# Kernel optimization log

Measured on AMD Instinct MI355X. Metric: run time of the kernel, lower is better.

## Reference

```python
import jax, jax.numpy as jnp
import numpy as np

N = 20000   # nodes
E = 200000  # directed edges (~kNN k=5, bidirectional)
IN = 256    # in_channels
D = 512     # projected_channels = in_channels * 2
NEG_SLOPE = 0.2


def _ln(x, g, b):
    mu = x.mean(-1, keepdims=True)
    var = ((x - mu) ** 2).mean(-1, keepdims=True)
    return (x - mu) * jax.lax.rsqrt(var + 1e-5) * g + b


def _gat(x, src, dst, W, a_s, a_d, bias, concat):
    # PyG GATConv: linear -> per-edge leaky-relu attention -> segment softmax over dst -> scatter-add
    n = x.shape[0]
    H, C = a_s.shape
    h = (x @ W).reshape(n, H, C)                      # [N,H,C]
    as_n = jnp.einsum('nhc,hc->nh', h, a_s)           # alpha contribution of src node
    ad_n = jnp.einsum('nhc,hc->nh', h, a_d)           # alpha contribution of dst node
    e = jax.nn.leaky_relu(as_n[src] + ad_n[dst], negative_slope=NEG_SLOPE)  # [E,H]
    m = jax.ops.segment_max(e, dst, num_segments=n)   # stable softmax per dst (self-loops => every dst nonempty)
    ex = jnp.exp(e - m[dst])
    den = jax.ops.segment_sum(ex, dst, num_segments=n)
    alpha = ex / den[dst]                             # [E,H]
    out = jax.ops.segment_sum(h[src] * alpha[:, :, None], dst, num_segments=n)  # [N,H,C]
    out = out.reshape(n, H * C) if concat else out.mean(axis=1)
    return out + bias


def setup_inputs() -> dict:
    key = jax.random.key(0)
    ks = jax.random.split(key, 40)
    x = jax.random.normal(ks[0], (N, IN), jnp.float32)
    src = jax.random.randint(ks[1], (E,), 0, N)
    off = jax.random.randint(ks[2], (E,), 1, N)
    dst = (src + off) % N                              # guarantees src != dst
    edge_index = jnp.stack([src, dst]).astype(jnp.int64)

    def p(k, shape, fan):
        return (jax.random.normal(k, shape, jnp.float32) / np.float32(np.sqrt(fan)))

    inp = {
        'x': x, 'edge_index': edge_index,
        'proj_W': p(ks[3], (IN, D), IN), 'proj_b': jnp.zeros((D,), jnp.float32),
        'blk_norm_g': jnp.ones((3, D), jnp.float32), 'blk_norm_b': jnp.zeros((3, D), jnp.float32),
        'g1_W': p(ks[4], (3, D, D), D), 'g1_as': p(ks[5], (3, 4, 128), 128), 'g1_ad': p(ks[6], (3, 4, 128), 128),
        'g1_b': jnp.zeros((3, D), jnp.float32),
        'g2_W': p(ks[7], (3, D, 128), D), 'g2_as': p(ks[8], (3, 2, 64), 64), 'g2_ad': p(ks[9], (3, 2, 64), 64),
        'g2_b': jnp.zeros((3, 128), jnp.float32),
        'uni_W': p(ks[10], (3, 640, D), 640), 'uni_b': jnp.zeros((3, D), jnp.float32),
        'fin_g': jnp.ones((D,), jnp.float32), 'fin_b': jnp.zeros((D,), jnp.float32),
        'fg_W': p(ks[11], (D, 8 * 128), D), 'fg_as': p(ks[12], (8, 128), 128), 'fg_ad': p(ks[13], (8, 128), 128),
        'fg_b': jnp.zeros((128,), jnp.float32),
    }
    return inp


def reference(x, edge_index, proj_W, proj_b, blk_norm_g, blk_norm_b,
              g1_W, g1_as, g1_ad, g1_b, g2_W, g2_as, g2_ad, g2_b,
              uni_W, uni_b, fin_g, fin_b, fg_W, fg_as, fg_ad, fg_b):
    n = x.shape[0]
    loops = jnp.arange(n, dtype=edge_index.dtype)
    src = jnp.concatenate([edge_index[0], loops])     # add_self_loops (PyG default)
    dst = jnp.concatenate([edge_index[1], loops])

    x = jax.nn.elu(x @ proj_W + proj_b)
    for i in range(3):
        res = x
        xn = _ln(x, blk_norm_g[i], blk_norm_b[i])
        o1 = _gat(xn, src, dst, g1_W[i], g1_as[i], g1_ad[i], g1_b[i], True)
        o2 = _gat(xn, src, dst, g2_W[i], g2_as[i], g2_ad[i], g2_b[i], True)
        xc = jax.nn.elu(jnp.concatenate([o1, o2], axis=-1))
        x = res + xc @ uni_W[i] + uni_b[i]
        x = jax.nn.elu(x)
    x = _ln(x, fin_g, fin_b)
    return _gat(x, src, dst, fg_W, fg_as, fg_ad, fg_b, False)  # heads=8, concat=False -> mean
```

## Files before the change

### kernel.cpp

```cpp
#include <hip/hip_runtime.h>
#include <math.h>

#define NN 20000
#define EDGES 200000

using short8  = __attribute__((ext_vector_type(8))) short;
using short4v = __attribute__((ext_vector_type(4))) short;
using f32x4   = __attribute__((ext_vector_type(4))) float;
typedef unsigned short ushortT;
typedef unsigned int uintT;

__device__ __forceinline__ ushortT f2bfu(float x) {
  union { float f; unsigned u; } c; c.f = x;
  unsigned r = c.u + 0x7FFFu + ((c.u >> 16) & 1u);
  return (ushortT)(r >> 16);
}
__device__ __forceinline__ float bflo(uintT u) {
  union { unsigned i; float f; } c; c.i = u << 16; return c.f;
}
__device__ __forceinline__ float bfhi(uintT u) {
  union { unsigned i; float f; } c; c.i = u & 0xFFFF0000u; return c.f;
}
__device__ __forceinline__ float elu_f(float v) { return v > 0.f ? v : (expf(v) - 1.f); }

__device__ __forceinline__ void acc8(float* acc, uint4 u, float a) {
  acc[0] += a * bflo(u.x); acc[1] += a * bfhi(u.x);
  acc[2] += a * bflo(u.y); acc[3] += a * bfhi(u.y);
  acc[4] += a * bflo(u.z); acc[5] += a * bfhi(u.z);
  acc[6] += a * bflo(u.w); acc[7] += a * bfhi(u.w);
}

__global__ void k_hist(const int* __restrict__ ei, int* __restrict__ cnt) {
  int i = blockIdx.x * 256 + threadIdx.x;
  const int EE = EDGES + NN;
  if (i >= EE) return;
  int d = (i < EDGES) ? ei[EDGES + i] : (i - EDGES);
  atomicAdd(&cnt[d], 1);
}

__global__ __launch_bounds__(256) void k_scan1(const int* __restrict__ cnt,
                                               int* __restrict__ bsum, int n) {
  int b = blockIdx.x, t = threadIdx.x, i = b * 256 + t;
  int v = (i < n) ? cnt[i] : 0;
#pragma unroll
  for (int off = 32; off > 0; off >>= 1) v += __shfl_down(v, off);
  __shared__ int s[4];
  if ((t & 63) == 0) s[t >> 6] = v;
  __syncthreads();
  if (t == 0) bsum[b] = s[0] + s[1] + s[2] + s[3];
}

__global__ void k_scan2(const int* __restrict__ bsum, int* __restrict__ boff,
                        int nb, int* __restrict__ ptr, int n) {
  if (threadIdx.x == 0) {
    int acc = 0;
    for (int b = 0; b < nb; ++b) { boff[b] = acc; acc += bsum[b]; }
    ptr[n] = acc;
  }
}

__global__ __launch_bounds__(256) void k_scan3(const int* __restrict__ cnt,
                                               const int* __restrict__ boff,
                                               int* __restrict__ ptr,
                                               int* __restrict__ cursor, int n) {
  __shared__ int sd[256];
  int b = blockIdx.x, t = threadIdx.x, i = b * 256 + t;
  int v = (i < n) ? cnt[i] : 0;
  sd[t] = v;
  __syncthreads();
  for (int off = 1; off < 256; off <<= 1) {
    int a = (t >= off) ? sd[t - off] : 0;
    __syncthreads();
    sd[t] += a;
    __syncthreads();
  }
  if (i < n) {
    int p = boff[b] + sd[t] - v;
    ptr[i] = p;
    cursor[i] = p;
  }
}

__global__ void k_scatter(const int* __restrict__ ei, int* __restrict__ cursor,
                          int* __restrict__ ssrc) {
  int i = blockIdx.x * 256 + threadIdx.x;
  const int EE = EDGES + NN;
  if (i >= EE) return;
  int s, d;
  if (i < EDGES) { s = ei[i]; d = ei[EDGES + i]; }
  else           { s = i - EDGES; d = s; }
  int pos = atomicAdd(&cursor[d], 1);
  ssrc[pos] = s;
}

struct CvtDesc { const float* src; ushortT* dst; int K; int N; int t0; };
struct CvtArgs { CvtDesc d[11]; };

__global__ __launch_bounds__(256) void k_cvtT(CvtArgs a) {
  __shared__ float tile[32][33];
  int b = blockIdx.x;
  int mi = 0;
#pragma unroll
  for (int i = 1; i < 11; ++i)
    if (b >= a.d[i].t0) mi = i;
  CvtDesc dd = a.d[mi];
  int tb = b - dd.t0;
  int tnc = dd.N / 32;
  int tk = tb / tnc, tn = tb % tnc;
  int t = threadIdx.x;
  {
    int r = t >> 3, c4 = (t & 7) * 4;
    float4 v = *reinterpret_cast<const float4*>(&dd.src[(size_t)(tk * 32 + r) * dd.N + tn * 32 + c4]);
    tile[r][c4 + 0] = v.x; tile[r][c4 + 1] = v.y; tile[r][c4 + 2] = v.z; tile[r][c4 + 3] = v.w;
  }
  __syncthreads();
  {
    int n = t >> 3, k4 = (t & 7) * 4;
    short4v s;
    s.x = (short)f2bfu(tile[k4 + 0][n]);
    s.y = (short)f2bfu(tile[k4 + 1][n]);
    s.z = (short)f2bfu(tile[k4 + 2][n]);
    s.w = (short)f2bfu(tile[k4 + 3][n]);
    *reinterpret_cast<short4v*>(&dd.dst[(size_t)(tn * 32 + n) * dd.K + tk * 32 + k4]) = s;
  }
}

__global__ void k_cvtX(const float* __restrict__ in, ushortT* __restrict__ out, int n4) {
  int i = blockIdx.x * 256 + threadIdx.x;
  if (i >= n4) return;
  float4 v = reinterpret_cast<const float4*>(in)[i];
  short4v s;
  s.x = (short)f2bfu(v.x); s.y = (short)f2bfu(v.y);
  s.z = (short)f2bfu(v.z); s.w = (short)f2bfu(v.w);
  reinterpret_cast<short4v*>(out)[i] = s;
}

__global__ __launch_bounds__(256) void k_ln(const float* __restrict__ in,
                                            const float* __restrict__ g,
                                            const float* __restrict__ b,
                                            ushortT* __restrict__ out) {
  int row = blockIdx.x, t = threadIdx.x;
  const float* r = in + (size_t)row * 512;
  float v0 = r[t], v1 = r[t + 256];
  __shared__ float red[4];
  int w = t >> 6, lane = t & 63;
  float s = v0 + v1;
#pragma unroll
  for (int off = 32; off > 0; off >>= 1) s += __shfl_down(s, off);
  if (lane == 0) red[w] = s;
  __syncthreads();
  float mu = (red[0] + red[1] + red[2] + red[3]) * (1.f / 512.f);
  float d0 = v0 - mu, d1 = v1 - mu;
  float vs = d0 * d0 + d1 * d1;
#pragma unroll
  for (int off = 32; off > 0; off >>= 1) vs += __shfl_down(vs, off);
  __syncthreads();
  if (lane == 0) red[w] = vs;
  __syncthreads();
  float var = (red[0] + red[1] + red[2] + red[3]) * (1.f / 512.f);
  float rs = rsqrtf(var + 1e-5f);
  ushortT* o = out + (size_t)row * 512;
  o[t]       = f2bfu(d0 * rs * g[t]       + b[t]);
  o[t + 256] = f2bfu(d1 * rs * g[t + 256] + b[t + 256]);
}

template <int EPI, bool OUTBF16, int NB>
__global__ __launch_bounds__(256) void k_gemm(const ushortT* __restrict__ A,
                                              const ushortT* __restrict__ Wt,
                                              const float* __restrict__ bias,
                                              const float* __restrict__ res,
                                              void* __restrict__ Outv,
                                              int M, int N, int K) {
  __shared__ short As[128][40];
  __shared__ short Bs[128][40];
  int b = blockIdx.x;
  int x = b & 7, g = b >> 3;
  int mt = x + 8 * (g / NB);
  int nt = g % NB;
  int m0 = mt * 128, n0 = nt * 128;
  if (m0 >= M) return;
  int t = threadIdx.x;
  int w = t >> 6, lane = t & 63;
  int wm = w >> 1, wn = w & 1;
  int lr = lane & 15, lk = (lane >> 4) * 8;
  int sr = t >> 2, sc = (t & 3) * 8;
  int ga0 = m0 + sr, ga1 = m0 + sr + 64;
  const short8 z8 = {};

  short8 vA0, vA1, vB0, vB1;
  {
    vA0 = (ga0 < M) ? *reinterpret_cast<const short8*>(&A[(size_t)ga0 * K + sc]) : z8;
    vA1 = (ga1 < M) ? *reinterpret_cast<const short8*>(&A[(size_t)ga1 * K + sc]) : z8;
    vB0 = *reinterpret_cast<const short8*>(&Wt[(size_t)(n0 + sr) * K + sc]);
    vB1 = *reinterpret_cast<const short8*>(&Wt[(size_t)(n0 + sr + 64) * K + sc]);
  }
  f32x4 acc[4][4] = {};
  for (int k0 = 0; k0 < K; k0 += 32) {
    *reinterpret_cast<short8*>(&As[sr][sc]) = vA0;
    *reinterpret_cast<short8*>(&As[sr + 64][sc]) = vA1;
    *reinterpret_cast<short8*>(&Bs[sr][sc]) = vB0;
    *reinterpret_cast<short8*>(&Bs[sr + 64][sc]) = vB1;
    __syncthreads();
    int k1 = k0 + 32;
    if (k1 < K) {
      vA0 = (ga0 < M) ? *reinterpret_cast<const short8*>(&A[(size_t)ga0 * K + k1 + sc]) : z8;
      vA1 = (ga1 < M) ? *reinterpret_cast<const short8*>(&A[(size_t)ga1 * K + k1 + sc]) : z8;
      vB0 = *reinterpret_cast<const short8*>(&Wt[(size_t)(n0 + sr) * K + k1 + sc]);
      vB1 = *reinterpret_cast<const short8*>(&Wt[(size_t)(n0 + sr + 64) * K + k1 + sc]);
    }
    short8 af[4], bf[4];
#pragma unroll
    for (int m = 0; m < 4; ++m)
      af[m] = *reinterpret_cast<const short8*>(&As[wm * 64 + m * 16 + lr][lk]);
#pragma unroll
    for (int n = 0; n < 4; ++n)
      bf[n] = *reinterpret_cast<const short8*>(&Bs[wn * 64 + n * 16 + lr][lk]);
#pragma unroll
    for (int m = 0; m < 4; ++m)
#pragma unroll
      for (int n = 0; n < 4; ++n)
        acc[m][n] = __builtin_amdgcn_mfma_f32_16x16x32_bf16(af[m], bf[n], acc[m][n], 0, 0, 0);
    __syncthreads();
  }
#pragma unroll
  for (int m = 0; m < 4; ++m) {
#pragma unroll
    for (int n = 0; n < 4; ++n) {
#pragma unroll
      for (int j = 0; j < 4; ++j) {
        int row = wm * 64 + m * 16 + (lane >> 4) * 4 + j;
        int col = wn * 64 + n * 16 + lr;
        int gr = m0 + row, gc = n0 + col;
        if (gr < M) {
          float v = acc[m][n][j];
          if (EPI >= 1) v += bias[gc];
          if (EPI == 2) v += res[(size_t)gr * N + gc];
          if (EPI >= 1) v = elu_f(v);
          if (OUTBF16) ((ushortT*)Outv)[(size_t)gr * N + gc] = f2bfu(v);
          else         ((float*)Outv)[(size_t)gr * N + gc] = v;
        }
      }
    }
  }
}

__global__ __launch_bounds__(384) void k_att_blk(const ushortT* __restrict__ h,
                                                 const float* __restrict__ w1s,
                                                 const float* __restrict__ w1d,
                                                 const float* __restrict__ w2s,
                                                 const float* __restrict__ w2d,
                                                 float* __restrict__ as_n,
                                                 float* __restrict__ ad_n) {
  int n = blockIdx.x;
  int hh = threadIdx.x >> 6, lane = threadIdx.x & 63;
  float s = 0.f, d = 0.f;
  if (hh < 4) {
    int c = lane * 2;
    uintT u = *reinterpret_cast<const uintT*>(&h[(size_t)n * 640 + hh * 128 + c]);
    float lo = bflo(u), hi = bfhi(u);
    s = lo * w1s[hh * 128 + c] + hi * w1s[hh * 128 + c + 1];
    d = lo * w1d[hh * 128 + c] + hi * w1d[hh * 128 + c + 1];
  } else if (lane < 32) {
    int hb = hh - 4;
    int c = lane * 2;
    uintT u = *reinterpret_cast<const uintT*>(&h[(size_t)n * 640 + 512 + hb * 64 + c]);
    float lo = bflo(u), hi = bfhi(u);
    s = lo * w2s[hb * 64 + c] + hi * w2s[hb * 64 + c + 1];
    d = lo * w2d[hb * 64 + c] + hi * w2d[hb * 64 + c + 1];
  }
#pragma unroll
  for (int o = 32; o > 0; o >>= 1) {
    s += __shfl_down(s, o);
    d += __shfl_down(d, o);
  }
  if (lane == 0) {
    as_n[n * 6 + hh] = s;
    ad_n[n * 6 + hh] = d;
  }
}

template <int H, int C>
__global__ void k_att(const ushortT* __restrict__ h, int rs, int off,
                      const float* __restrict__ as_w,
                      const float* __restrict__ ad_w, float* __restrict__ as_n,
                      float* __restrict__ ad_n) {
  int n = blockIdx.x;
  int hh = threadIdx.x >> 6;
  int lane = threadIdx.x & 63;
  float s = 0.f, d = 0.f;
  if (C == 128 || lane < 32) {
    int c = lane * 2;
    uintT u = *reinterpret_cast<const uintT*>(&h[(size_t)n * rs + off + hh * C + c]);
    float lo = bflo(u), hi = bfhi(u);
    s = lo * as_w[hh * C + c] + hi * as_w[hh * C + c + 1];
    d = lo * ad_w[hh * C + c] + hi * ad_w[hh * C + c + 1];
  }
#pragma unroll
  for (int o = 32; o > 0; o >>= 1) {
    s += __shfl_down(s, o);
    d += __shfl_down(d, o);
  }
  if (lane == 0) {
    as_n[n * H + hh] = s;
    ad_n[n * H + hh] = d;
  }
}

template <int H>
__global__ __launch_bounds__(256) void k_soft16(const float* __restrict__ as_n,
                                                const float* __restrict__ ad_n,
                                                const int* __restrict__ rowptr,
                                                const int* __restrict__ ssrc,
                                                float* __restrict__ alpha) {
  int t = threadIdx.x;
  int grp16 = t >> 4;
  int l = t & 15;
  int dnode = blockIdx.x * 16 + grp16;
  int e0 = rowptr[dnode], deg = rowptr[dnode + 1] - e0;
  float adv[H], m[H], den[H];
#pragma unroll
  for (int hh = 0; hh < H; ++hh) {
    adv[hh] = ad_n[dnode * H + hh];
    m[hh] = -INFINITY;
    den[hh] = 0.f;
  }
  for (int base = 0; base < deg; base += 16) {
    int j = base + l;
    float e[H];
    if (j < deg) {
      int s = ssrc[e0 + j];
#pragma unroll
      for (int hh = 0; hh < H; ++hh) {
        float v = as_n[s * H + hh] + adv[hh];
        e[hh] = v > 0.f ? v : 0.2f * v;
      }
    } else {
#pragma unroll
      for (int hh = 0; hh < H; ++hh) e[hh] = -INFINITY;
    }
#pragma unroll
    for (int hh = 0; hh < H; ++hh) {
      float v = e[hh];
#pragma unroll
      for (int o = 8; o > 0; o >>= 1) v = fmaxf(v, __shfl_xor(v, o, 16));
      m[hh] = fmaxf(m[hh], v);
    }
  }
  for (int base = 0; base < deg; base += 16) {
    int j = base + l;
    float p[H];
    if (j < deg) {
      int s = ssrc[e0 + j];
#pragma unroll
      for (int hh = 0; hh < H; ++hh) {
        float v = as_n[s * H + hh] + adv[hh];
        v = v > 0.f ? v : 0.2f * v;
        p[hh] = expf(v - m[hh]);
        alpha[(size_t)(e0 + j) * H + hh] = p[hh];
      }
    } else {
#pragma unroll
      for (int hh = 0; hh < H; ++hh) p[hh] = 0.f;
    }
#pragma unroll
    for (int hh = 0; hh < H; ++hh) {
      float v = p[hh];
#pragma unroll
      for (int o = 8; o > 0; o >>= 1) v += __shfl_xor(v, o, 16);
      den[hh] += v;
    }
  }
  float rden[H];
#pragma unroll
  for (int hh = 0; hh < H; ++hh) rden[hh] = 1.f / den[hh];
  for (int base = 0; base < deg; base += 16) {
    int j = base + l;
    if (j < deg) {
#pragma unroll
      for (int hh = 0; hh < H; ++hh)
        alpha[(size_t)(e0 + j) * H + hh] *= rden[hh];
    }
  }
}

__global__ __launch_bounds__(320) void k_agg_blk(const ushortT* __restrict__ h,
                                                 const float* __restrict__ alpha,
                                                 const int* __restrict__ rowptr,
                                                 const int* __restrict__ ssrc,
                                                 const float* __restrict__ b1,
                                                 const float* __restrict__ b2,
                                                 ushortT* __restrict__ out) {
  int dnode = blockIdx.x;
  int t = threadIdx.x;
  int grp = t / 80;
  int r = t - grp * 80;
  int ch0 = r * 8;
  int head = (ch0 < 512) ? (ch0 >> 7) : (4 + ((ch0 - 512) >> 6));
  int e0 = rowptr[dnode], deg = rowptr[dnode + 1] - e0;
  float acc[8] = {};
  __shared__ float s_alpha[64 * 6];
  __shared__ int s_src[64];
  __shared__ float s_part[4][640];
  for (int base = 0; base < deg; base += 64) {
    int cnt = min(64, deg - base);
    __syncthreads();
    for (int tix = t; tix < cnt * 6; tix += 320)
      s_alpha[tix] = alpha[(size_t)(e0 + base) * 6 + tix];
    for (int tix = t; tix < cnt; tix += 320)
      s_src[tix] = ssrc[e0 + base + tix];
    __syncthreads();
    int jj = grp;
    for (; jj + 4 < cnt; jj += 8) {
      int sA = s_src[jj], sB = s_src[jj + 4];
      uint4 uA = *reinterpret_cast<const uint4*>(h + (size_t)sA * 640 + ch0);
      uint4 uB = *reinterpret_cast<const uint4*>(h + (size_t)sB * 640 + ch0);
      acc8(acc, uA, s_alpha[jj * 6 + head]);
      acc8(acc, uB, s_alpha[(jj + 4) * 6 + head]);
    }
    if (jj < cnt) {
      int sA = s_src[jj];
      uint4 uA = *reinterpret_cast<const uint4*>(h + (size_t)sA * 640 + ch0);
      acc8(acc, uA, s_alpha[jj * 6 + head]);
    }
  }
  __syncthreads();
#pragma unroll
  for (int q = 0; q < 8; ++q) s_part[grp][ch0 + q] = acc[q];
  __syncthreads();
  {
    int ch = t * 2;
    float v0 = s_part[0][ch] + s_part[1][ch] + s_part[2][ch] + s_part[3][ch];
    float v1 = s_part[0][ch + 1] + s_part[1][ch + 1] + s_part[2][ch + 1] + s_part[3][ch + 1];
    v0 += (ch < 512) ? b1[ch] : b2[ch - 512];
    v1 += (ch < 512) ? b1[ch + 1] : b2[ch - 511];
    v0 = elu_f(v0); v1 = elu_f(v1);
    uintT o = (uintT)f2bfu(v0) | ((uintT)f2bfu(v1) << 16);
    *reinterpret_cast<uintT*>(&out[(size_t)dnode * 640 + ch]) = o;
  }
}

__global__ __launch_bounds__(256) void k_agg_mean(
    const ushortT* __restrict__ h, const float* __restrict__ alpha,
    const int* __restrict__ rowptr, const int* __restrict__ ssrc,
    const float* __restrict__ bias, float* __restrict__ out) {
  int dnode = blockIdx.x;
  int t = threadIdx.x;
  int grp = t >> 7;
  int r = t & 127;
  int head = r >> 4;
  int e0 = rowptr[dnode], deg = rowptr[dnode + 1] - e0;
  float acc[8] = {};
  __shared__ float s_alpha[64 * 8];
  __shared__ int s_src[64];
  __shared__ float s_part[2][1024];
  for (int base = 0; base < deg; base += 64) {
    int cnt = min(64, deg - base);
    __syncthreads();
    for (int tix = t; tix < cnt * 8; tix += 256)
      s_alpha[tix] = alpha[(size_t)(e0 + base) * 8 + tix];
    for (int tix = t; tix < cnt; tix += 256)
      s_src[tix] = ssrc[e0 + base + tix];
    __syncthreads();
    int jj = grp;
    for (; jj + 2 < cnt; jj += 4) {
      int sA = s_src[jj], sB = s_src[jj + 2];
      uint4 uA = *reinterpret_cast<const uint4*>(h + (size_t)sA * 1024 + r * 8);
      uint4 uB = *reinterpret_cast<const uint4*>(h + (size_t)sB * 1024 + r * 8);
      acc8(acc, uA, s_alpha[jj * 8 + head]);
      acc8(acc, uB, s_alpha[(jj + 2) * 8 + head]);
    }
    if (jj < cnt) {
      int sA = s_src[jj];
      uint4 uA = *reinterpret_cast<const uint4*>(h + (size_t)sA * 1024 + r * 8);
      acc8(acc, uA, s_alpha[jj * 8 + head]);
    }
  }
  __syncthreads();
#pragma unroll
  for (int q = 0; q < 8; ++q) s_part[grp][r * 8 + q] = acc[q];
  __syncthreads();
  if (t < 128) {
    float v = 0.f;
#pragma unroll
    for (int hh = 0; hh < 8; ++hh)
      v += s_part[0][hh * 128 + t] + s_part[1][hh * 128 + t];
    out[(size_t)dnode * 128 + t] = v * 0.125f + bias[t];
  }
}

extern "C" void kernel_launch(void* const* d_in, const int* in_sizes, int n_in,
                              void* d_out, int out_size, void* d_ws, size_t ws_size,
                              hipStream_t stream) {
  const float* x_in   = (const float*)d_in[0];
  const int*   ei     = (const int*)d_in[1];
  const float* proj_W = (const float*)d_in[2];
  const float* proj_b = (const float*)d_in[3];
  const float* bng    = (const float*)d_in[4];
  const float* bnb    = (const float*)d_in[5];
  const float* g1W    = (const float*)d_in[6];
  const float* g1as   = (const float*)d_in[7];
  const float* g1ad   = (const float*)d_in[8];
  const float* g1b    = (const float*)d_in[9];
  const float* g2W    = (const float*)d_in[10];
  const float* g2as   = (const float*)d_in[11];
  const float* g2ad   = (const float*)d_in[12];
  const float* g2b    = (const float*)d_in[13];
  const float* uniW   = (const float*)d_in[14];
  const float* unib   = (const float*)d_in[15];
  const float* fing   = (const float*)d_in[16];
  const float* finb   = (const float*)d_in[17];
  const float* fgW    = (const float*)d_in[18];
  const float* fgas   = (const float*)d_in[19];
  const float* fgad   = (const float*)d_in[20];
  const float* fgb    = (const float*)d_in[21];

  const int EE = EDGES + NN;
  char* ws = (char*)d_ws;
  size_t off = 0;
  auto alloc = [&](size_t bytes) -> void* {
    void* p = ws + off;
    off += (bytes + 255) & ~(size_t)255;
    return p;
  };
  float*   xA    = (float*)alloc((size_t)NN * 512 * 4);
  float*   xB    = (float*)alloc((size_t)NN * 512 * 4);
  ushortT* xn    = (ushortT*)alloc((size_t)NN * 512 * 2);
  ushortT* xinb  = (ushortT*)alloc((size_t)NN * 256 * 2);
  ushortT* hcat  = (ushortT*)alloc((size_t)NN * 640 * 2);
  ushortT* xc    = (ushortT*)alloc((size_t)NN * 640 * 2);
  float*   asb   = (float*)alloc((size_t)NN * 8 * 4);
  float*   adb   = (float*)alloc((size_t)NN * 8 * 4);
  float*   alphab= (float*)alloc((size_t)EE * 8 * 4);
  ushortT* projT = (ushortT*)alloc((size_t)512 * 256 * 2);
  ushortT* gcatT = (ushortT*)alloc((size_t)3 * 640 * 512 * 2);
  ushortT* uniT  = (ushortT*)alloc((size_t)3 * 512 * 640 * 2);
  ushortT* fgT   = (ushortT*)alloc((size_t)1024 * 512 * 2);
  int* cnt    = (int*)alloc((size_t)NN * 4);
  int* ptr    = (int*)alloc((size_t)(NN + 1) * 4);
  int* cursor = (int*)alloc((size_t)NN * 4);
  int* ssrc   = (int*)alloc((size_t)EE * 4);
  int* bsum   = (int*)alloc((size_t)128 * 4);
  int* boff   = (int*)alloc((size_t)128 * 4);
  ushortT* hf = hcat;

  const int NB79 = (NN + 255) / 256;

  hipMemsetAsync(cnt, 0, (size_t)NN * 4, stream);
  k_hist<<<(EE + 255) / 256, 256, 0, stream>>>(ei, cnt);
  k_scan1<<<NB79, 256, 0, stream>>>(cnt, bsum, NN);
  k_scan2<<<1, 64, 0, stream>>>(bsum, boff, NB79, ptr, NN);
  k_scan3<<<NB79, 256, 0, stream>>>(cnt, boff, ptr, cursor, NN);
  k_scatter<<<(EE + 255) / 256, 256, 0, stream>>>(ei, cursor, ssrc);

  {
    CvtArgs a;
    int t0 = 0;
    auto add = [&](int idx, const float* s, ushortT* d, int K, int N) {
      a.d[idx] = { s, d, K, N, t0 };
      t0 += (K / 32) * (N / 32);
    };
    add(0, proj_W, projT, 256, 512);
    for (int i = 0; i < 3; ++i)
      add(1 + i, g1W + (size_t)i * 512 * 512, gcatT + (size_t)i * 640 * 512, 512, 512);
    for (int i = 0; i < 3; ++i)
      add(4 + i, g2W + (size_t)i * 512 * 128, gcatT + (size_t)i * 640 * 512 + 512 * 512, 512, 128);
    for (int i = 0; i < 3; ++i)
      add(7 + i, uniW + (size_t)i * 640 * 512, uniT + (size_t)i * 512 * 640, 640, 512);
    add(10, fgW, fgT, 512, 1024);
    k_cvtT<<<t0, 256, 0, stream>>>(a);
  }
  k_cvtX<<<(NN * 256 / 4 + 255) / 256, 256, 0, stream>>>(x_in, xinb, NN * 256 / 4);

  const int GMP = 160;

  k_gemm<1, false, 4><<<GMP * 4, 256, 0, stream>>>(xinb, projT, proj_b, nullptr, xA, NN, 512, 256);

  float* cur = xA;
  float* alt = xB;
  for (int i = 0; i < 3; ++i) {
    k_ln<<<NN, 256, 0, stream>>>(cur, bng + i * 512, bnb + i * 512, xn);
    k_gemm<0, true, 5><<<GMP * 5, 256, 0, stream>>>(xn, gcatT + (size_t)i * 640 * 512, nullptr, nullptr, hcat, NN, 640, 512);
    k_att_blk<<<NN, 384, 0, stream>>>(hcat, g1as + i * 512, g1ad + i * 512,
                                      g2as + i * 128, g2ad + i * 128, asb, adb);
    k_soft16<6><<<NN / 16, 256, 0, stream>>>(asb, adb, ptr, ssrc, alphab);
    k_agg_blk<<<NN, 320, 0, stream>>>(hcat, alphab, ptr, ssrc, g1b + i * 512, g2b + i * 128, xc);
    k_gemm<2, false, 4><<<GMP * 4, 256, 0, stream>>>(xc, uniT + (size_t)i * 512 * 640, unib + i * 512, cur, alt, NN, 512, 640);
    float* tmp = cur; cur = alt; alt = tmp;
  }

  k_ln<<<NN, 256, 0, stream>>>(cur, fing, finb, xn);
  k_gemm<0, true, 8><<<GMP * 8, 256, 0, stream>>>(xn, fgT, nullptr, nullptr, hf, NN, 1024, 512);
  k_att<8, 128><<<NN, 512, 0, stream>>>(hf, 1024, 0, fgas, fgad, asb, adb);
  k_soft16<8><<<NN / 16, 256, 0, stream>>>(asb, adb, ptr, ssrc, alphab);
  k_agg_mean<<<NN, 256, 0, stream>>>(hf, alphab, ptr, ssrc, fgb, (float*)d_out);
}
```

Measured before the change: 736.3 us.

## Defer softmax normalization into aggregation and unroll gather loops four-deep

The softmax kernel no longer rescales alpha in a second pass over edges. It writes per-node reciprocal denominators, and the aggregation kernels multiply the summed result by them after the reduction. This removes a read-modify-write pass over the alpha array. The gather loops in both aggregation kernels are unrolled to four independent loads with predication to raise memory-level parallelism, and k_agg_mean grows from 256 to 512 threads with a larger shared partial buffer. Predicated-off loads still fetch a clamped row, and the larger block uses more shared memory, which may lower occupancy.

```diff
diff --git a/kernel.cpp b/kernel.cpp
--- a/kernel.cpp
+++ b/kernel.cpp
@@ -311,7 +311,8 @@
                                                 const float* __restrict__ ad_n,
                                                 const int* __restrict__ rowptr,
                                                 const int* __restrict__ ssrc,
-                                                float* __restrict__ alpha) {
+                                                float* __restrict__ alpha,
+                                                float* __restrict__ rden_out) {
   int t = threadIdx.x;
   int grp16 = t >> 4;
   int l = t & 15;
@@ -370,21 +371,16 @@
       den[hh] += v;
     }
   }
-  float rden[H];
-#pragma unroll
-  for (int hh = 0; hh < H; ++hh) rden[hh] = 1.f / den[hh];
-  for (int base = 0; base < deg; base += 16) {
-    int j = base + l;
-    if (j < deg) {
-#pragma unroll
-      for (int hh = 0; hh < H; ++hh)
-        alpha[(size_t)(e0 + j) * H + hh] *= rden[hh];
-    }
+  if (l == 0) {
+#pragma unroll
+    for (int hh = 0; hh < H; ++hh)
+      rden_out[dnode * H + hh] = 1.f / den[hh];
   }
 }
 
 __global__ __launch_bounds__(320) void k_agg_blk(const ushortT* __restrict__ h,
                                                  const float* __restrict__ alpha,
+                                                 const float* __restrict__ rden,
                                                  const int* __restrict__ rowptr,
                                                  const int* __restrict__ ssrc,
                                                  const float* __restrict__ b1,
@@ -409,18 +405,26 @@
     for (int tix = t; tix < cnt; tix += 320)
       s_src[tix] = ssrc[e0 + base + tix];
     __syncthreads();
-    int jj = grp;
-    for (; jj + 4 < cnt; jj += 8) {
-      int sA = s_src[jj], sB = s_src[jj + 4];
+    int cl = cnt - 1;
+    for (int jj = grp; jj < cnt; jj += 16) {
+      int j1 = jj + 4, j2 = jj + 8, j3 = jj + 12;
+      bool q1 = j1 < cnt, q2 = j2 < cnt, q3 = j3 < cnt;
+      int sA = s_src[jj];
+      int sB = s_src[q1 ? j1 : cl];
+      int sC = s_src[q2 ? j2 : cl];
+      int sD = s_src[q3 ? j3 : cl];
+      float aA = s_alpha[jj * 6 + head];
+      float aB = q1 ? s_alpha[j1 * 6 + head] : 0.f;
+      float aC = q2 ? s_alpha[j2 * 6 + head] : 0.f;
+      float aD = q3 ? s_alpha[j3 * 6 + head] : 0.f;
       uint4 uA = *reinterpret_cast<const uint4*>(h + (size_t)sA * 640 + ch0);
       uint4 uB = *reinterpret_cast<const uint4*>(h + (size_t)sB * 640 + ch0);
-      acc8(acc, uA, s_alpha[jj * 6 + head]);
-      acc8(acc, uB, s_alpha[(jj + 4) * 6 + head]);
-    }
-    if (jj < cnt) {
-      int sA = s_src[jj];
-      uint4 uA = *reinterpret_cast<const uint4*>(h + (size_t)sA * 640 + ch0);
-      acc8(acc, uA, s_alpha[jj * 6 + head]);
+      uint4 uC = *reinterpret_cast<const uint4*>(h + (size_t)sC * 640 + ch0);
+      uint4 uD = *reinterpret_cast<const uint4*>(h + (size_t)sD * 640 + ch0);
+      acc8(acc, uA, aA);
+      if (q1) acc8(acc, uB, aB);
+      if (q2) acc8(acc, uC, aC);
+      if (q3) acc8(acc, uD, aD);
     }
   }
   __syncthreads();
@@ -429,8 +433,11 @@
   __syncthreads();
   {
     int ch = t * 2;
+    int hh = (ch < 512) ? (ch >> 7) : (4 + ((ch - 512) >> 6));
+    float rd = rden[dnode * 6 + hh];
     float v0 = s_part[0][ch] + s_part[1][ch] + s_part[2][ch] + s_part[3][ch];
     float v1 = s_part[0][ch + 1] + s_part[1][ch + 1] + s_part[2][ch + 1] + s_part[3][ch + 1];
+    v0 *= rd; v1 *= rd;
     v0 += (ch < 512) ? b1[ch] : b2[ch - 512];
     v1 += (ch < 512) ? b1[ch + 1] : b2[ch - 511];
     v0 = elu_f(v0); v1 = elu_f(v1);
@@ -439,8 +446,9 @@
   }
 }
 
-__global__ __launch_bounds__(256) void k_agg_mean(
+__global__ __launch_bounds__(512) void k_agg_mean(
     const ushortT* __restrict__ h, const float* __restrict__ alpha,
+    const float* __restrict__ rden,
     const int* __restrict__ rowptr, const int* __restrict__ ssrc,
     const float* __restrict__ bias, float* __restrict__ out) {
   int dnode = blockIdx.x;
@@ -452,27 +460,35 @@
   float acc[8] = {};
   __shared__ float s_alpha[64 * 8];
   __shared__ int s_src[64];
-  __shared__ float s_part[2][1024];
+  __shared__ float s_part[4][1024];
   for (int base = 0; base < deg; base += 64) {
     int cnt = min(64, deg - base);
     __syncthreads();
-    for (int tix = t; tix < cnt * 8; tix += 256)
+    for (int tix = t; tix < cnt * 8; tix += 512)
       s_alpha[tix] = alpha[(size_t)(e0 + base) * 8 + tix];
-    for (int tix = t; tix < cnt; tix += 256)
+    for (int tix = t; tix < cnt; tix += 512)
       s_src[tix] = ssrc[e0 + base + tix];
     __syncthreads();
-    int jj = grp;
-    for (; jj + 2 < cnt; jj += 4) {
-      int sA = s_src[jj], sB = s_src[jj + 2];
+    int cl = cnt - 1;
+    for (int jj = grp; jj < cnt; jj += 16) {
+      int j1 = jj + 4, j2 = jj + 8, j3 = jj + 12;
+      bool q1 = j1 < cnt, q2 = j2 < cnt, q3 = j3 < cnt;
+      int sA = s_src[jj];
+      int sB = s_src[q1 ? j1 : cl];
+      int sC = s_src[q2 ? j2 : cl];
+      int sD = s_src[q3 ? j3 : cl];
+      float aA = s_alpha[jj * 8 + head];
+      float aB = q1 ? s_alpha[j1 * 8 + head] : 0.f;
+      float aC = q2 ? s_alpha[j2 * 8 + head] : 0.f;
+      float aD = q3 ? s_alpha[j3 * 8 + head] : 0.f;
       uint4 uA = *reinterpret_cast<const uint4*>(h + (size_t)sA * 1024 + r * 8);
       uint4 uB = *reinterpret_cast<const uint4*>(h + (size_t)sB * 1024 + r * 8);
-      acc8(acc, uA, s_alpha[jj * 8 + head]);
-      acc8(acc, uB, s_alpha[(jj + 2) * 8 + head]);
-    }
-    if (jj < cnt) {
-      int sA = s_src[jj];
-      uint4 uA = *reinterpret_cast<const uint4*>(h + (size_t)sA * 1024 + r * 8);
-      acc8(acc, uA, s_alpha[jj * 8 + head]);
+      uint4 uC = *reinterpret_cast<const uint4*>(h + (size_t)sC * 1024 + r * 8);
+      uint4 uD = *reinterpret_cast<const uint4*>(h + (size_t)sD * 1024 + r * 8);
+      acc8(acc, uA, aA);
+      if (q1) acc8(acc, uB, aB);
+      if (q2) acc8(acc, uC, aC);
+      if (q3) acc8(acc, uD, aD);
     }
   }
   __syncthreads();
@@ -482,8 +498,11 @@
   if (t < 128) {
     float v = 0.f;
 #pragma unroll
-    for (int hh = 0; hh < 8; ++hh)
-      v += s_part[0][hh * 128 + t] + s_part[1][hh * 128 + t];
+    for (int hh = 0; hh < 8; ++hh) {
+      float ph = s_part[0][hh * 128 + t] + s_part[1][hh * 128 + t]
+               + s_part[2][hh * 128 + t] + s_part[3][hh * 128 + t];
+      v += ph * rden[dnode * 8 + hh];
+    }
     out[(size_t)dnode * 128 + t] = v * 0.125f + bias[t];
   }
 }
@@ -530,6 +549,7 @@
   ushortT* xc    = (ushortT*)alloc((size_t)NN * 640 * 2);
   float*   asb   = (float*)alloc((size_t)NN * 8 * 4);
   float*   adb   = (float*)alloc((size_t)NN * 8 * 4);
+  float*   denb  = (float*)alloc((size_t)NN * 8 * 4);
   float*   alphab= (float*)alloc((size_t)EE * 8 * 4);
   ushortT* projT = (ushortT*)alloc((size_t)512 * 256 * 2);
   ushortT* gcatT = (ushortT*)alloc((size_t)3 * 640 * 512 * 2);
@@ -582,8 +602,8 @@
     k_gemm<0, true, 5><<<GMP * 5, 256, 0, stream>>>(xn, gcatT + (size_t)i * 640 * 512, nullptr, nullptr, hcat, NN, 640, 512);
     k_att_blk<<<NN, 384, 0, stream>>>(hcat, g1as + i * 512, g1ad + i * 512,
                                       g2as + i * 128, g2ad + i * 128, asb, adb);
-    k_soft16<6><<<NN / 16, 256, 0, stream>>>(asb, adb, ptr, ssrc, alphab);
-    k_agg_blk<<<NN, 320, 0, stream>>>(hcat, alphab, ptr, ssrc, g1b + i * 512, g2b + i * 128, xc);
+    k_soft16<6><<<NN / 16, 256, 0, stream>>>(asb, adb, ptr, ssrc, alphab, denb);
+    k_agg_blk<<<NN, 320, 0, stream>>>(hcat, alphab, denb, ptr, ssrc, g1b + i * 512, g2b + i * 128, xc);
     k_gemm<2, false, 4><<<GMP * 4, 256, 0, stream>>>(xc, uniT + (size_t)i * 512 * 640, unib + i * 512, cur, alt, NN, 512, 640);
     float* tmp = cur; cur = alt; alt = tmp;
   }
@@ -591,6 +611,6 @@
   k_ln<<<NN, 256, 0, stream>>>(cur, fing, finb, xn);
   k_gemm<0, true, 8><<<GMP * 8, 256, 0, stream>>>(xn, fgT, nullptr, nullptr, hf, NN, 1024, 512);
   k_att<8, 128><<<NN, 512, 0, stream>>>(hf, 1024, 0, fgas, fgad, asb, adb);
-  k_soft16<8><<<NN / 16, 256, 0, stream>>>(asb, adb, ptr, ssrc, alphab);
-  k_agg_mean<<<NN, 256, 0, stream>>>(hf, alphab, ptr, ssrc, fgb, (float*)d_out);
-}
+  k_soft16<8><<<NN / 16, 256, 0, stream>>>(asb, adb, ptr, ssrc, alphab, denb);
+  k_agg_mean<<<NN, 512, 0, stream>>>(hf, alphab, denb, ptr, ssrc, fgb, (float*)d_out);
+}
```

New measurement: 748.3 us. Within noise of the previous version (+1.6%).

## Load GEMM tiles directly to LDS and defer softmax normalization to aggregation

Applied to the files above, without the earlier changes.

The GEMM main loop now uses global_load_lds to move A and B tiles straight into unpadded LDS, dropping register staging, the software prefetch and the row bounds checks. The A-operand buffers are padded to a multiple of the tile height to allow that. The softmax kernel no longer makes a second pass over alpha to divide by the denominator; it stores per-node reciprocal denominators, and the aggregation kernels multiply by them. This saves the alpha read-modify-write traffic and register staging, but loses prefetch overlap and may add LDS bank conflicts.

```diff
diff --git a/kernel.cpp b/kernel.cpp
--- a/kernel.cpp
+++ b/kernel.cpp
@@ -3,6 +3,7 @@
 
 #define NN 20000
 #define EDGES 200000
+#define MPAD 20096
 
 using short8  = __attribute__((ext_vector_type(8))) short;
 using short4v = __attribute__((ext_vector_type(4))) short;
@@ -29,6 +30,11 @@
   acc[4] += a * bflo(u.z); acc[5] += a * bfhi(u.z);
   acc[6] += a * bflo(u.w); acc[7] += a * bfhi(u.w);
 }
+
+#define GLDS16(gp, lp)                                                  \
+  __builtin_amdgcn_global_load_lds(                                     \
+      (const __attribute__((address_space(1))) void*)(gp),              \
+      (__attribute__((address_space(3))) void*)(lp), 16, 0, 0)
 
 __global__ void k_hist(const int* __restrict__ ei, int* __restrict__ cnt) {
   int i = blockIdx.x * 256 + threadIdx.x;
@@ -171,8 +177,8 @@
                                               const float* __restrict__ res,
                                               void* __restrict__ Outv,
                                               int M, int N, int K) {
-  __shared__ short As[128][40];
-  __shared__ short Bs[128][40];
+  __shared__ short As[128][32];
+  __shared__ short Bs[128][32];
   int b = blockIdx.x;
   int x = b & 7, g = b >> 3;
   int mt = x + 8 * (g / NB);
@@ -183,31 +189,22 @@
   int w = t >> 6, lane = t & 63;
   int wm = w >> 1, wn = w & 1;
   int lr = lane & 15, lk = (lane >> 4) * 8;
-  int sr = t >> 2, sc = (t & 3) * 8;
-  int ga0 = m0 + sr, ga1 = m0 + sr + 64;
-  const short8 z8 = {};
-
-  short8 vA0, vA1, vB0, vB1;
-  {
-    vA0 = (ga0 < M) ? *reinterpret_cast<const short8*>(&A[(size_t)ga0 * K + sc]) : z8;
-    vA1 = (ga1 < M) ? *reinterpret_cast<const short8*>(&A[(size_t)ga1 * K + sc]) : z8;
-    vB0 = *reinterpret_cast<const short8*>(&Wt[(size_t)(n0 + sr) * K + sc]);
-    vB1 = *reinterpret_cast<const short8*>(&Wt[(size_t)(n0 + sr + 64) * K + sc]);
-  }
+  int srow = w * 32 + (lane >> 2);
+  int scol = (lane & 3) * 8;
+  const ushortT* gA = &A[(size_t)(m0 + srow) * K + scol];
+  const ushortT* gB = &Wt[(size_t)(n0 + srow) * K + scol];
+  short* lA0 = &As[w * 32][0];
+  short* lA1 = &As[w * 32 + 16][0];
+  short* lB0 = &Bs[w * 32][0];
+  short* lB1 = &Bs[w * 32 + 16][0];
+
   f32x4 acc[4][4] = {};
   for (int k0 = 0; k0 < K; k0 += 32) {
-    *reinterpret_cast<short8*>(&As[sr][sc]) = vA0;
-    *reinterpret_cast<short8*>(&As[sr + 64][sc]) = vA1;
-    *reinterpret_cast<short8*>(&Bs[sr][sc]) = vB0;
-    *reinterpret_cast<short8*>(&Bs[sr + 64][sc]) = vB1;
-    __syncthreads();
-    int k1 = k0 + 32;
-    if (k1 < K) {
-      vA0 = (ga0 < M) ? *reinterpret_cast<const short8*>(&A[(size_t)ga0 * K + k1 + sc]) : z8;
-      vA1 = (ga1 < M) ? *reinterpret_cast<const short8*>(&A[(size_t)ga1 * K + k1 + sc]) : z8;
-      vB0 = *reinterpret_cast<const short8*>(&Wt[(size_t)(n0 + sr) * K + k1 + sc]);
-      vB1 = *reinterpret_cast<const short8*>(&Wt[(size_t)(n0 + sr + 64) * K + k1 + sc]);
-    }
+    GLDS16(gA + k0, lA0);
+    GLDS16(gA + k0 + (size_t)16 * K, lA1);
+    GLDS16(gB + k0, lB0);
+    GLDS16(gB + k0 + (size_t)16 * K, lB1);
+    __syncthreads();
     short8 af[4], bf[4];
 #pragma unroll
     for (int m = 0; m < 4; ++m)
@@ -311,7 +308,8 @@
                                                 const float* __restrict__ ad_n,
                                                 const int* __restrict__ rowptr,
                                                 const int* __restrict__ ssrc,
-                                                float* __restrict__ alpha) {
+                                                float* __restrict__ alpha,
+                                                float* __restrict__ rden_out) {
   int t = threadIdx.x;
   int grp16 = t >> 4;
   int l = t & 15;
@@ -370,21 +368,16 @@
       den[hh] += v;
     }
   }
-  float rden[H];
-#pragma unroll
-  for (int hh = 0; hh < H; ++hh) rden[hh] = 1.f / den[hh];
-  for (int base = 0; base < deg; base += 16) {
-    int j = base + l;
-    if (j < deg) {
-#pragma unroll
-      for (int hh = 0; hh < H; ++hh)
-        alpha[(size_t)(e0 + j) * H + hh] *= rden[hh];
-    }
+  if (l == 0) {
+#pragma unroll
+    for (int hh = 0; hh < H; ++hh)
+      rden_out[dnode * H + hh] = 1.f / den[hh];
   }
 }
 
 __global__ __launch_bounds__(320) void k_agg_blk(const ushortT* __restrict__ h,
                                                  const float* __restrict__ alpha,
+                                                 const float* __restrict__ rden,
                                                  const int* __restrict__ rowptr,
                                                  const int* __restrict__ ssrc,
                                                  const float* __restrict__ b1,
@@ -429,8 +422,11 @@
   __syncthreads();
   {
     int ch = t * 2;
+    int hh = (ch < 512) ? (ch >> 7) : (4 + ((ch - 512) >> 6));
+    float rd = rden[dnode * 6 + hh];
     float v0 = s_part[0][ch] + s_part[1][ch] + s_part[2][ch] + s_part[3][ch];
     float v1 = s_part[0][ch + 1] + s_part[1][ch + 1] + s_part[2][ch + 1] + s_part[3][ch + 1];
+    v0 *= rd; v1 *= rd;
     v0 += (ch < 512) ? b1[ch] : b2[ch - 512];
     v1 += (ch < 512) ? b1[ch + 1] : b2[ch - 511];
     v0 = elu_f(v0); v1 = elu_f(v1);
@@ -441,6 +437,7 @@
 
 __global__ __launch_bounds__(256) void k_agg_mean(
     const ushortT* __restrict__ h, const float* __restrict__ alpha,
+    const float* __restrict__ rden,
     const int* __restrict__ rowptr, const int* __restrict__ ssrc,
     const float* __restrict__ bias, float* __restrict__ out) {
   int dnode = blockIdx.x;
@@ -482,8 +479,10 @@
   if (t < 128) {
     float v = 0.f;
 #pragma unroll
-    for (int hh = 0; hh < 8; ++hh)
-      v += s_part[0][hh * 128 + t] + s_part[1][hh * 128 + t];
+    for (int hh = 0; hh < 8; ++hh) {
+      float ph = s_part[0][hh * 128 + t] + s_part[1][hh * 128 + t];
+      v += ph * rden[dnode * 8 + hh];
+    }
     out[(size_t)dnode * 128 + t] = v * 0.125f + bias[t];
   }
 }
@@ -524,12 +523,13 @@
   };
   float*   xA    = (float*)alloc((size_t)NN * 512 * 4);
   float*   xB    = (float*)alloc((size_t)NN * 512 * 4);
-  ushortT* xn    = (ushortT*)alloc((size_t)NN * 512 * 2);
-  ushortT* xinb  = (ushortT*)alloc((size_t)NN * 256 * 2);
+  ushortT* xn    = (ushortT*)alloc((size_t)MPAD * 512 * 2);
+  ushortT* xinb  = (ushortT*)alloc((size_t)MPAD * 256 * 2);
   ushortT* hcat  = (ushortT*)alloc((size_t)NN * 640 * 2);
-  ushortT* xc    = (ushortT*)alloc((size_t)NN * 640 * 2);
+  ushortT* xc    = (ushortT*)alloc((size_t)MPAD * 640 * 2);
   float*   asb   = (float*)alloc((size_t)NN * 8 * 4);
   float*   adb   = (float*)alloc((size_t)NN * 8 * 4);
+  float*   denb  = (float*)alloc((size_t)NN * 8 * 4);
   float*   alphab= (float*)alloc((size_t)EE * 8 * 4);
   ushortT* projT = (ushortT*)alloc((size_t)512 * 256 * 2);
   ushortT* gcatT = (ushortT*)alloc((size_t)3 * 640 * 512 * 2);
@@ -582,8 +582,8 @@
     k_gemm<0, true, 5><<<GMP * 5, 256, 0, stream>>>(xn, gcatT + (size_t)i * 640 * 512, nullptr, nullptr, hcat, NN, 640, 512);
     k_att_blk<<<NN, 384, 0, stream>>>(hcat, g1as + i * 512, g1ad + i * 512,
                                       g2as + i * 128, g2ad + i * 128, asb, adb);
-    k_soft16<6><<<NN / 16, 256, 0, stream>>>(asb, adb, ptr, ssrc, alphab);
-    k_agg_blk<<<NN, 320, 0, stream>>>(hcat, alphab, ptr, ssrc, g1b + i * 512, g2b + i * 128, xc);
+    k_soft16<6><<<NN / 16, 256, 0, stream>>>(asb, adb, ptr, ssrc, alphab, denb);
+    k_agg_blk<<<NN, 320, 0, stream>>>(hcat, alphab, denb, ptr, ssrc, g1b + i * 512, g2b + i * 128, xc);
     k_gemm<2, false, 4><<<GMP * 4, 256, 0, stream>>>(xc, uniT + (size_t)i * 512 * 640, unib + i * 512, cur, alt, NN, 512, 640);
     float* tmp = cur; cur = alt; alt = tmp;
   }
@@ -591,6 +591,6 @@
   k_ln<<<NN, 256, 0, stream>>>(cur, fing, finb, xn);
   k_gemm<0, true, 8><<<GMP * 8, 256, 0, stream>>>(xn, fgT, nullptr, nullptr, hf, NN, 1024, 512);
   k_att<8, 128><<<NN, 512, 0, stream>>>(hf, 1024, 0, fgas, fgad, asb, adb);
-  k_soft16<8><<<NN / 16, 256, 0, stream>>>(asb, adb, ptr, ssrc, alphab);
-  k_agg_mean<<<NN, 256, 0, stream>>>(hf, alphab, ptr, ssrc, fgb, (float*)d_out);
-}
+  k_soft16<8><<<NN / 16, 256, 0, stream>>>(asb, adb, ptr, ssrc, alphab, denb);
+  k_agg_mean<<<NN, 256, 0, stream>>>(hf, alphab, denb, ptr, ssrc, fgb, (float*)d_out);
+}
```

Result: slower. 759.4 us (+3.1%).
